# Kernel optimization log

Measured on AMD Instinct MI355X. Metric: run time of the kernel, lower is better.

The kernel has to match this reference:

```python
import jax, jax.numpy as jnp
import numpy as np

KS = 7       # neighborhood kernel size (fixed in __init__)
HEADS = 8    # num_heads (fixed in __init__)
LN_EPS = 1e-5


def _nbr_idx(L, k):
    # NATTEN-style clamped window: window start shifts inward at borders (no padding)
    starts = jnp.clip(jnp.arange(L) - k // 2, 0, L - k)
    idx = starts[:, None] + jnp.arange(k)            # [L, k] absolute neighbor coords
    rel = idx - jnp.arange(L)[:, None] + (k - 1)     # [L, k] rel-pos-bias index in [0, 2k-2]
    return idx, rel


def _na2d(x, qkv_w, qkv_b, proj_w, proj_b, rpb):
    # x: [B, H, W, C]  -> neighborhood attention with clamped 7x7 windows
    B, H, W, C = x.shape
    hd = C // HEADS
    qkv = x @ qkv_w.T + qkv_b                        # [B,H,W,3C]
    q, k, v = jnp.split(qkv, 3, axis=-1)
    q = q.reshape(B, H, W, HEADS, hd) * (hd ** -0.5)
    k = k.reshape(B, H, W, HEADS, hd)
    v = v.reshape(B, H, W, HEADS, hd)
    ri, rri = _nbr_idx(H, KS)                        # [H,KS]
    ci, rci = _nbr_idx(W, KS)                        # [W,KS]
    # gather neighborhoods: [B,H,W,KS,KS,heads,hd]
    kn = k[:, ri[:, None, :, None], ci[None, :, None, :]]
    vn = v[:, ri[:, None, :, None], ci[None, :, None, :]]
    scores = jnp.einsum('bijhd,bijpqhd->bhijpq', q, kn)   # [B,heads,H,W,KS,KS]
    bias = rpb[:, rri[:, None, :, None], rci[None, :, None, :]]  # [heads,H,W,KS,KS]
    scores = scores + bias[None]
    attn = jax.nn.softmax(scores.reshape(B, HEADS, H, W, KS * KS), axis=-1)
    vn = vn.reshape(B, H, W, KS * KS, HEADS, hd)
    out = jnp.einsum('bhijp,bijphd->bijhd', attn, vn)      # [B,H,W,heads,hd]
    out = out.reshape(B, H, W, C)
    return out @ proj_w.T + proj_b


def _layernorm(x, g, b):
    mu = jnp.mean(x, axis=-1, keepdims=True)
    var = jnp.mean((x - mu) ** 2, axis=-1, keepdims=True)
    return (x - mu) * jax.lax.rsqrt(var + LN_EPS) * g + b


def setup_inputs() -> dict:
    key = jax.random.key(0)
    ks = jax.random.split(key, 4)
    B, T, H, W, C = 2, 8, 48, 48, 64
    return {
        'q': jax.random.normal(ks[0], (B, T, H, W, C), dtype=jnp.float32),
        'qkv_w': jax.random.normal(ks[1], (3 * C, C), dtype=jnp.float32) * 0.02,
        'qkv_b': jnp.zeros((3 * C,), jnp.float32),
        'proj_w': jax.random.normal(ks[2], (C, C), dtype=jnp.float32) * 0.02,
        'proj_b': jnp.zeros((C,), jnp.float32),
        'rpb': jax.random.normal(ks[3], (HEADS, 2 * KS - 1, 2 * KS - 1), dtype=jnp.float32) * 0.02,
        'ln_g': jnp.ones((C,), jnp.float32),
        'ln_b': jnp.zeros((C,), jnp.float32),
    }


def reference(q, qkv_w, qkv_b, proj_w, proj_b, rpb, ln_g, ln_b):
    B, T, H, W, C = q.shape
    x = q.reshape(B * T, H, W, C)                    # '(b t) h w c'
    x = _na2d(x, qkv_w, qkv_b, proj_w, proj_b, rpb)  # wPT path
    x = x.reshape(B, T, H, W, C)
    return _layernorm(x, ln_g, ln_b)                 # norm_q; wGC=False
```

## Files before the change

### kernel.cpp

```cpp
#include <hip/hip_runtime.h>
#include <hip/hip_bf16.h>

#define IH   48
#define IW   48
#define CH   64
#define KS   7
#define LN_EPS 1e-5f
#define QSCALE 0.35355339059327373f
#define L2E    1.4426950408889634f

#define TS   8
#define HS   14
#define HP   196
#define KVS  136
#define AOS  72

typedef __bf16 bf16_t;
typedef bf16_t bf16x8 __attribute__((ext_vector_type(8)));
typedef float  f32x4  __attribute__((ext_vector_type(4)));
typedef float  f32x2  __attribute__((ext_vector_type(2)));

__device__ __forceinline__ float bflo(unsigned u) { union { unsigned i; float f; } v; v.i = u << 16; return v.f; }
__device__ __forceinline__ float bfhi(unsigned u) { union { unsigned i; float f; } v; v.i = u & 0xffff0000u; return v.f; }
__device__ __forceinline__ f32x2 unp2(unsigned u) { f32x2 r; r.x = bflo(u); r.y = bfhi(u); return r; }

__device__ __forceinline__ float4 ldf4u(const float* p) {
    float4 r; __builtin_memcpy(&r, p, 16); return r;
}

__device__ __forceinline__ bf16x8 pack_bf16x8(float4 lo, float4 hi) {
    bf16x8 r;
    r[0] = (bf16_t)lo.x; r[1] = (bf16_t)lo.y; r[2] = (bf16_t)lo.z; r[3] = (bf16_t)lo.w;
    r[4] = (bf16_t)hi.x; r[5] = (bf16_t)hi.y; r[6] = (bf16_t)hi.z; r[7] = (bf16_t)hi.w;
    return r;
}

__global__ __launch_bounds__(512, 4) void fused_na_kernel(
        const float* __restrict__ x,
        const float* __restrict__ w,
        const float* __restrict__ b,
        const float* __restrict__ rpb,
        const float* __restrict__ pw,
        const float* __restrict__ pb,
        const float* __restrict__ g,
        const float* __restrict__ beta,
        float* __restrict__ out) {
    __shared__ __align__(16) __hip_bfloat16 kv[HP * KVS];
    __shared__ __align__(16) __hip_bfloat16 qao[64 * AOS];

    const int blk  = blockIdx.x;
    const int n    = blk & 15;
    const int tile = blk >> 4;
    const int i0   = (tile / 6) * TS;
    const int j0   = (tile % 6) * TS;
    int h0 = i0 - 3; h0 = h0 < 0 ? 0 : (h0 > IH - HS ? IH - HS : h0);
    int w0 = j0 - 3; w0 = w0 < 0 ? 0 : (w0 > IW - HS ? IW - HS : w0);
    const int tid = threadIdx.x;
    const size_t img = (size_t)n * (IH * IW);

    {
        const int wv = tid >> 6;
        const int l  = tid & 63;
        const int m  = l & 15;
        const int kg = l >> 4;

        if (wv < 4) {
            const int ch_base = m * 4;
            const float4 bias4 = *(const float4*)(b + ch_base);
            bf16x8 wb0[4], wb1[4];
            #pragma unroll
            for (int t = 0; t < 4; ++t) {
                const float* wr_ = w + (size_t)(ch_base + t) * CH + kg * 8;
                wb0[t] = pack_bf16x8(*(const float4*)(wr_),      *(const float4*)(wr_ + 4));
                wb1[t] = pack_bf16x8(*(const float4*)(wr_ + 32), *(const float4*)(wr_ + 36));
            }
            const int px = wv * 16 + m;
            const int hr = i0 + (px >> 3);
            const int wc = j0 + (px & 7);
            const float* xr = x + (img + hr * IW + wc) * CH + kg * 8;
            const bf16x8 a0 = pack_bf16x8(*(const float4*)(xr),      *(const float4*)(xr + 4));
            const bf16x8 a1 = pack_bf16x8(*(const float4*)(xr + 32), *(const float4*)(xr + 36));
            float val[4][4];
            #pragma unroll
            for (int t = 0; t < 4; ++t) {
                f32x4 acc = {0.f, 0.f, 0.f, 0.f};
                acc = __builtin_amdgcn_mfma_f32_16x16x32_bf16(a0, wb0[t], acc, 0, 0, 0);
                acc = __builtin_amdgcn_mfma_f32_16x16x32_bf16(a1, wb1[t], acc, 0, 0, 0);
                const float bias = (t == 0) ? bias4.x : (t == 1) ? bias4.y : (t == 2) ? bias4.z : bias4.w;
                #pragma unroll
                for (int rr = 0; rr < 4; ++rr) val[t][rr] = (acc[rr] + bias) * (QSCALE * L2E);
            }
            #pragma unroll
            for (int rr = 0; rr < 4; ++rr) {
                const int pix = wv * 16 + kg * 4 + rr;
                union { ushort4 u; __hip_bfloat16 hh[4]; } pk;
                #pragma unroll
                for (int t = 0; t < 4; ++t) pk.hh[t] = __float2bfloat16(val[t][rr]);
                *reinterpret_cast<ushort4*>(qao + pix * AOS + ch_base) = pk.u;
            }
        }

        {
            const int grp = 1 + (wv >> 2);
            const int ch_base = grp * 64 + m * 4;
            const float4 bias4 = *(const float4*)(b + ch_base);
            bf16x8 wb0[4], wb1[4];
            #pragma unroll
            for (int t = 0; t < 4; ++t) {
                const float* wr_ = w + (size_t)(ch_base + t) * CH + kg * 8;
                wb0[t] = pack_bf16x8(*(const float4*)(wr_),      *(const float4*)(wr_ + 4));
                wb1[t] = pack_bf16x8(*(const float4*)(wr_ + 32), *(const float4*)(wr_ + 36));
            }
            for (int mt = wv & 3; mt < 13; mt += 4) {
                int hp = mt * 16 + m; if (hp > HP - 1) hp = HP - 1;
                const int hr = h0 + hp / HS;
                const int wc = w0 + hp % HS;
                const float* xr = x + (img + hr * IW + wc) * CH + kg * 8;
                const bf16x8 a0 = pack_bf16x8(*(const float4*)(xr),      *(const float4*)(xr + 4));
                const bf16x8 a1 = pack_bf16x8(*(const float4*)(xr + 32), *(const float4*)(xr + 36));
                float val[4][4];
                #pragma unroll
                for (int t = 0; t < 4; ++t) {
                    f32x4 acc = {0.f, 0.f, 0.f, 0.f};
                    acc = __builtin_amdgcn_mfma_f32_16x16x32_bf16(a0, wb0[t], acc, 0, 0, 0);
                    acc = __builtin_amdgcn_mfma_f32_16x16x32_bf16(a1, wb1[t], acc, 0, 0, 0);
                    const float bias = (t == 0) ? bias4.x : (t == 1) ? bias4.y : (t == 2) ? bias4.z : bias4.w;
                    #pragma unroll
                    for (int rr = 0; rr < 4; ++rr) val[t][rr] = acc[rr] + bias;
                }
                #pragma unroll
                for (int rr = 0; rr < 4; ++rr) {
                    const int pix = mt * 16 + kg * 4 + rr;
                    if (pix < HP) {
                        union { ushort4 u; __hip_bfloat16 hh[4]; } pk;
                        #pragma unroll
                        for (int t = 0; t < 4; ++t) pk.hh[t] = __float2bfloat16(val[t][rr]);
                        *reinterpret_cast<ushort4*>(kv + pix * KVS + (grp - 1) * 64 + m * 4) = pk.u;
                    }
                }
            }
        }
    }
    __syncthreads();

    {
        const int h  = tid & 7;
        const int px = tid >> 3;
        const int i  = i0 + (px >> 3);
        const int j  = j0 + (px & 7);

        f32x2 q0[4];
        {
            const uint4 u = *reinterpret_cast<const uint4*>(qao + px * AOS + h * 8);
            q0[0] = unp2(u.x); q0[1] = unp2(u.y); q0[2] = unp2(u.z); q0[3] = unp2(u.w);
        }
        __syncthreads();

        int si = i - 3;  si = si < 0 ? 0 : (si > IH - KS ? IH - KS : si);
        int sj = j - 3;  sj = sj < 0 ? 0 : (sj > IW - KS ? IW - KS : sj);
        const float* rpc = rpb + h * (2*KS-1) * (2*KS-1)
                               + (si - i + (KS-1)) * (2*KS-1) + (sj - j + (KS-1));
        const __hip_bfloat16* kbase = kv + ((si - h0) * HS + (sj - w0)) * KVS + h * 8;

        float lr = 0.f;
        f32x2 a[4];
        #pragma unroll
        for (int d = 0; d < 4; ++d) a[d] = (f32x2){0.f, 0.f};

        #pragma unroll
        for (int p = 0; p < KS; ++p) {
            const __hip_bfloat16* row = kbase + p * (HS * KVS);
            uint4 kb[KS], vb[KS];
            #pragma unroll
            for (int qq = 0; qq < KS; ++qq) {
                kb[qq] = *reinterpret_cast<const uint4*>(row + qq * KVS);
                vb[qq] = *reinterpret_cast<const uint4*>(row + qq * KVS + 64);
            }
            const float* rr = rpc + p * (2*KS-1);
            const float4 ba = ldf4u(rr);
            const float4 bb = ldf4u(rr + 3);

            float s[KS];
            #pragma unroll
            for (int qq = 0; qq < KS; ++qq) {
                const f32x2 k0 = unp2(kb[qq].x), k1 = unp2(kb[qq].y);
                const f32x2 k2 = unp2(kb[qq].z), k3 = unp2(kb[qq].w);
                f32x2 t = q0[0]*k0 + q0[1]*k1 + q0[2]*k2 + q0[3]*k3;
                s[qq] = t.x + t.y;
            }
            float e[KS];
            e[0] = __builtin_amdgcn_exp2f(fmaf(ba.x, L2E, s[0]));
            e[1] = __builtin_amdgcn_exp2f(fmaf(ba.y, L2E, s[1]));
            e[2] = __builtin_amdgcn_exp2f(fmaf(ba.z, L2E, s[2]));
            e[3] = __builtin_amdgcn_exp2f(fmaf(ba.w, L2E, s[3]));
            e[4] = __builtin_amdgcn_exp2f(fmaf(bb.y, L2E, s[4]));
            e[5] = __builtin_amdgcn_exp2f(fmaf(bb.z, L2E, s[5]));
            e[6] = __builtin_amdgcn_exp2f(fmaf(bb.w, L2E, s[6]));

            #pragma unroll
            for (int qq = 0; qq < KS; ++qq) {
                const f32x2 v0 = unp2(vb[qq].x), v1 = unp2(vb[qq].y);
                const f32x2 v2 = unp2(vb[qq].z), v3 = unp2(vb[qq].w);
                lr += e[qq];
                a[0] += e[qq] * v0; a[1] += e[qq] * v1;
                a[2] += e[qq] * v2; a[3] += e[qq] * v3;
            }
        }
        const float inv = 1.f / lr;
        union { uint4 u; __hip_bfloat16 hh[8]; } pk;
        #pragma unroll
        for (int d = 0; d < 4; ++d) {
            pk.hh[2*d]   = __float2bfloat16(a[d].x * inv);
            pk.hh[2*d+1] = __float2bfloat16(a[d].y * inv);
        }
        *reinterpret_cast<uint4*>(qao + px * AOS + h * 8) = pk.u;
    }
    __syncthreads();

    if ((tid >> 6) < 4) {
        const int wv = tid >> 6;
        const int l  = tid & 63;
        const int m  = l & 15;
        const int kg = l >> 4;

        const __hip_bfloat16* ar = qao + (wv * 16 + m) * AOS + kg * 8;
        const bf16x8 a0 = *reinterpret_cast<const bf16x8*>(ar);
        const bf16x8 a1 = *reinterpret_cast<const bf16x8*>(ar + 32);

        const int ch_base = m * 4;
        const float4 bias4 = *(const float4*)(pb + ch_base);

        float val[4][4];
        #pragma unroll
        for (int t = 0; t < 4; ++t) {
            const float* wr_ = pw + (size_t)(ch_base + t) * CH + kg * 8;
            const bf16x8 b0 = pack_bf16x8(*(const float4*)(wr_),      *(const float4*)(wr_ + 4));
            const bf16x8 b1 = pack_bf16x8(*(const float4*)(wr_ + 32), *(const float4*)(wr_ + 36));
            f32x4 acc = {0.f, 0.f, 0.f, 0.f};
            acc = __builtin_amdgcn_mfma_f32_16x16x32_bf16(a0, b0, acc, 0, 0, 0);
            acc = __builtin_amdgcn_mfma_f32_16x16x32_bf16(a1, b1, acc, 0, 0, 0);
            const float bias = (t == 0) ? bias4.x : (t == 1) ? bias4.y : (t == 2) ? bias4.z : bias4.w;
            #pragma unroll
            for (int r = 0; r < 4; ++r) val[t][r] = acc[r] + bias;
        }

        float sm[4];
        #pragma unroll
        for (int r = 0; r < 4; ++r) sm[r] = val[0][r] + val[1][r] + val[2][r] + val[3][r];
        #pragma unroll
        for (int mask = 1; mask <= 8; mask <<= 1) {
            #pragma unroll
            for (int r = 0; r < 4; ++r) sm[r] += __shfl_xor(sm[r], mask, 64);
        }
        float mu[4];
        #pragma unroll
        for (int r = 0; r < 4; ++r) mu[r] = sm[r] * (1.f / 64.f);

        float qs[4];
        #pragma unroll
        for (int r = 0; r < 4; ++r) {
            float aa = val[0][r] - mu[r], bq = val[1][r] - mu[r];
            float c  = val[2][r] - mu[r], d  = val[3][r] - mu[r];
            qs[r] = aa * aa + bq * bq + c * c + d * d;
        }
        #pragma unroll
        for (int mask = 1; mask <= 8; mask <<= 1) {
            #pragma unroll
            for (int r = 0; r < 4; ++r) qs[r] += __shfl_xor(qs[r], mask, 64);
        }
        float rs[4];
        #pragma unroll
        for (int r = 0; r < 4; ++r) rs[r] = rsqrtf(qs[r] * (1.f / 64.f) + LN_EPS);

        const float4 g4  = *(const float4*)(g + ch_base);
        const float4 be4 = *(const float4*)(beta + ch_base);
        #pragma unroll
        for (int r = 0; r < 4; ++r) {
            const int pl = wv * 16 + kg * 4 + r;
            const int gi = i0 + (pl >> 3), gj = j0 + (pl & 7);
            float4 o;
            o.x = (val[0][r] - mu[r]) * rs[r] * g4.x + be4.x;
            o.y = (val[1][r] - mu[r]) * rs[r] * g4.y + be4.y;
            o.z = (val[2][r] - mu[r]) * rs[r] * g4.z + be4.z;
            o.w = (val[3][r] - mu[r]) * rs[r] * g4.w + be4.w;
            *reinterpret_cast<float4*>(out + (img + gi * IW + gj) * CH + ch_base) = o;
        }
    }
}

extern "C" void kernel_launch(void* const* d_in, const int* in_sizes, int n_in,
                              void* d_out, int out_size, void* d_ws, size_t ws_size,
                              hipStream_t stream) {
    const float* x      = (const float*)d_in[0];
    const float* qkv_w  = (const float*)d_in[1];
    const float* qkv_b  = (const float*)d_in[2];
    const float* proj_w = (const float*)d_in[3];
    const float* proj_b = (const float*)d_in[4];
    const float* rpb    = (const float*)d_in[5];
    const float* ln_g   = (const float*)d_in[6];
    const float* ln_b   = (const float*)d_in[7];
    float* out = (float*)d_out;

    fused_na_kernel<<<576, 512, 0, stream>>>(x, qkv_w, qkv_b, rpb,
                                             proj_w, proj_b, ln_g, ln_b, out);
}
```

Before: 119.9 us.

## Retile to 6x12 output tiles with 576-thread blocks and LDS-staged rpb

Changes the spatial tile from 8x8 to 6x12 pixels, so the K/V halo grows from 14x14 to 12x18 while covering 72 outputs, which lowers halo recompute per output pixel. The grid becomes 512 blocks of 576 threads. A dedicated ninth wave computes Q while the other eight compute K/V, and the relative-position bias table is copied into shared memory instead of being read from global memory per neighbor row. The neighbor-row loop is no longer unrolled, and the projection and LayerNorm stage now uses five waves with padding guards, which adds some idle lanes and more LDS use per block.

```diff
diff --git a/kernel.cpp b/kernel.cpp
--- a/kernel.cpp
+++ b/kernel.cpp
@@ -9,11 +9,15 @@
 #define QSCALE 0.35355339059327373f
 #define L2E    1.4426950408889634f
 
-#define TS   8
-#define HS   14
-#define HP   196
+#define TSH  6
+#define TSW  12
+#define TPX  72
+#define HSH  12
+#define HSW  18
+#define HP   216
 #define KVS  136
 #define AOS  72
+#define RPBN 1352
 
 typedef __bf16 bf16_t;
 typedef bf16_t bf16x8 __attribute__((ext_vector_type(8)));
@@ -23,10 +27,6 @@
 __device__ __forceinline__ float bflo(unsigned u) { union { unsigned i; float f; } v; v.i = u << 16; return v.f; }
 __device__ __forceinline__ float bfhi(unsigned u) { union { unsigned i; float f; } v; v.i = u & 0xffff0000u; return v.f; }
 __device__ __forceinline__ f32x2 unp2(unsigned u) { f32x2 r; r.x = bflo(u); r.y = bfhi(u); return r; }
-
-__device__ __forceinline__ float4 ldf4u(const float* p) {
-    float4 r; __builtin_memcpy(&r, p, 16); return r;
-}
 
 __device__ __forceinline__ bf16x8 pack_bf16x8(float4 lo, float4 hi) {
     bf16x8 r;
@@ -35,7 +35,7 @@
     return r;
 }
 
-__global__ __launch_bounds__(512, 4) void fused_na_kernel(
+__global__ __launch_bounds__(576, 5) void fused_na_kernel(
         const float* __restrict__ x,
         const float* __restrict__ w,
         const float* __restrict__ b,
@@ -46,17 +46,20 @@
         const float* __restrict__ beta,
         float* __restrict__ out) {
     __shared__ __align__(16) __hip_bfloat16 kv[HP * KVS];
-    __shared__ __align__(16) __hip_bfloat16 qao[64 * AOS];
+    __shared__ __align__(16) __hip_bfloat16 qao[TPX * AOS];
+    __shared__ __align__(16) float rpbl[RPBN];
 
     const int blk  = blockIdx.x;
     const int n    = blk & 15;
     const int tile = blk >> 4;
-    const int i0   = (tile / 6) * TS;
-    const int j0   = (tile % 6) * TS;
-    int h0 = i0 - 3; h0 = h0 < 0 ? 0 : (h0 > IH - HS ? IH - HS : h0);
-    int w0 = j0 - 3; w0 = w0 < 0 ? 0 : (w0 > IW - HS ? IW - HS : w0);
+    const int i0   = (tile >> 2) * TSH;
+    const int j0   = (tile & 3) * TSW;
+    int h0 = i0 - 3; h0 = h0 < 0 ? 0 : (h0 > IH - HSH ? IH - HSH : h0);
+    int w0 = j0 - 3; w0 = w0 < 0 ? 0 : (w0 > IW - HSW ? IW - HSW : w0);
     const int tid = threadIdx.x;
     const size_t img = (size_t)n * (IH * IW);
+
+    for (int idx = tid; idx < RPBN; idx += 576) rpbl[idx] = rpb[idx];
 
     {
         const int wv = tid >> 6;
@@ -64,7 +67,7 @@
         const int m  = l & 15;
         const int kg = l >> 4;
 
-        if (wv < 4) {
+        if (wv == 8) {
             const int ch_base = m * 4;
             const float4 bias4 = *(const float4*)(b + ch_base);
             bf16x8 wb0[4], wb1[4];
@@ -74,34 +77,37 @@
                 wb0[t] = pack_bf16x8(*(const float4*)(wr_),      *(const float4*)(wr_ + 4));
                 wb1[t] = pack_bf16x8(*(const float4*)(wr_ + 32), *(const float4*)(wr_ + 36));
             }
-            const int px = wv * 16 + m;
-            const int hr = i0 + (px >> 3);
-            const int wc = j0 + (px & 7);
-            const float* xr = x + (img + hr * IW + wc) * CH + kg * 8;
-            const bf16x8 a0 = pack_bf16x8(*(const float4*)(xr),      *(const float4*)(xr + 4));
-            const bf16x8 a1 = pack_bf16x8(*(const float4*)(xr + 32), *(const float4*)(xr + 36));
-            float val[4][4];
-            #pragma unroll
-            for (int t = 0; t < 4; ++t) {
-                f32x4 acc = {0.f, 0.f, 0.f, 0.f};
-                acc = __builtin_amdgcn_mfma_f32_16x16x32_bf16(a0, wb0[t], acc, 0, 0, 0);
-                acc = __builtin_amdgcn_mfma_f32_16x16x32_bf16(a1, wb1[t], acc, 0, 0, 0);
-                const float bias = (t == 0) ? bias4.x : (t == 1) ? bias4.y : (t == 2) ? bias4.z : bias4.w;
+            for (int mt = 0; mt < 5; ++mt) {
+                int px = mt * 16 + m; if (px > TPX - 1) px = TPX - 1;
+                const int hr = i0 + px / TSW;
+                const int wc = j0 + px % TSW;
+                const float* xr = x + (img + hr * IW + wc) * CH + kg * 8;
+                const bf16x8 a0 = pack_bf16x8(*(const float4*)(xr),      *(const float4*)(xr + 4));
+                const bf16x8 a1 = pack_bf16x8(*(const float4*)(xr + 32), *(const float4*)(xr + 36));
+                float val[4][4];
                 #pragma unroll
-                for (int rr = 0; rr < 4; ++rr) val[t][rr] = (acc[rr] + bias) * (QSCALE * L2E);
-            }
-            #pragma unroll
-            for (int rr = 0; rr < 4; ++rr) {
-                const int pix = wv * 16 + kg * 4 + rr;
-                union { ushort4 u; __hip_bfloat16 hh[4]; } pk;
+                for (int t = 0; t < 4; ++t) {
+                    f32x4 acc = {0.f, 0.f, 0.f, 0.f};
+                    acc = __builtin_amdgcn_mfma_f32_16x16x32_bf16(a0, wb0[t], acc, 0, 0, 0);
+                    acc = __builtin_amdgcn_mfma_f32_16x16x32_bf16(a1, wb1[t], acc, 0, 0, 0);
+                    const float bias = (t == 0) ? bias4.x : (t == 1) ? bias4.y : (t == 2) ? bias4.z : bias4.w;
+                    #pragma unroll
+                    for (int rr = 0; rr < 4; ++rr) val[t][rr] = (acc[rr] + bias) * (QSCALE * L2E);
+                }
                 #pragma unroll
-                for (int t = 0; t < 4; ++t) pk.hh[t] = __float2bfloat16(val[t][rr]);
-                *reinterpret_cast<ushort4*>(qao + pix * AOS + ch_base) = pk.u;
-            }
-        }
-
-        {
+                for (int rr = 0; rr < 4; ++rr) {
+                    const int pix = mt * 16 + kg * 4 + rr;
+                    if (pix < TPX) {
+                        union { ushort4 u; __hip_bfloat16 hh[4]; } pk;
+                        #pragma unroll
+                        for (int t = 0; t < 4; ++t) pk.hh[t] = __float2bfloat16(val[t][rr]);
+                        *reinterpret_cast<ushort4*>(qao + pix * AOS + ch_base) = pk.u;
+                    }
+                }
+            }
+        } else {
             const int grp = 1 + (wv >> 2);
+            const int wg  = wv & 3;
             const int ch_base = grp * 64 + m * 4;
             const float4 bias4 = *(const float4*)(b + ch_base);
             bf16x8 wb0[4], wb1[4];
@@ -111,10 +117,10 @@
                 wb0[t] = pack_bf16x8(*(const float4*)(wr_),      *(const float4*)(wr_ + 4));
                 wb1[t] = pack_bf16x8(*(const float4*)(wr_ + 32), *(const float4*)(wr_ + 36));
             }
-            for (int mt = wv & 3; mt < 13; mt += 4) {
+            for (int mt = wg; mt < 14; mt += 4) {
                 int hp = mt * 16 + m; if (hp > HP - 1) hp = HP - 1;
-                const int hr = h0 + hp / HS;
-                const int wc = w0 + hp % HS;
+                const int hr = h0 + hp / HSW;
+                const int wc = w0 + hp % HSW;
                 const float* xr = x + (img + hr * IW + wc) * CH + kg * 8;
                 const bf16x8 a0 = pack_bf16x8(*(const float4*)(xr),      *(const float4*)(xr + 4));
                 const bf16x8 a1 = pack_bf16x8(*(const float4*)(xr + 32), *(const float4*)(xr + 36));
@@ -146,8 +152,8 @@
     {
         const int h  = tid & 7;
         const int px = tid >> 3;
-        const int i  = i0 + (px >> 3);
-        const int j  = j0 + (px & 7);
+        const int i  = i0 + px / TSW;
+        const int j  = j0 + px % TSW;
 
         f32x2 q0[4];
         {
@@ -158,27 +164,26 @@
 
         int si = i - 3;  si = si < 0 ? 0 : (si > IH - KS ? IH - KS : si);
         int sj = j - 3;  sj = sj < 0 ? 0 : (sj > IW - KS ? IW - KS : sj);
-        const float* rpc = rpb + h * (2*KS-1) * (2*KS-1)
-                               + (si - i + (KS-1)) * (2*KS-1) + (sj - j + (KS-1));
-        const __hip_bfloat16* kbase = kv + ((si - h0) * HS + (sj - w0)) * KVS + h * 8;
+        const float* rpc = rpbl + h * (2*KS-1) * (2*KS-1)
+                                + (si - i + (KS-1)) * (2*KS-1) + (sj - j + (KS-1));
+        const __hip_bfloat16* kbase = kv + ((si - h0) * HSW + (sj - w0)) * KVS + h * 8;
 
         float lr = 0.f;
         f32x2 a[4];
         #pragma unroll
         for (int d = 0; d < 4; ++d) a[d] = (f32x2){0.f, 0.f};
 
-        #pragma unroll
         for (int p = 0; p < KS; ++p) {
-            const __hip_bfloat16* row = kbase + p * (HS * KVS);
+            const __hip_bfloat16* row = kbase + p * (HSW * KVS);
             uint4 kb[KS], vb[KS];
             #pragma unroll
             for (int qq = 0; qq < KS; ++qq) {
                 kb[qq] = *reinterpret_cast<const uint4*>(row + qq * KVS);
                 vb[qq] = *reinterpret_cast<const uint4*>(row + qq * KVS + 64);
             }
-            const float* rr = rpc + p * (2*KS-1);
-            const float4 ba = ldf4u(rr);
-            const float4 bb = ldf4u(rr + 3);
+            float bl[KS];
+            #pragma unroll
+            for (int qq = 0; qq < KS; ++qq) bl[qq] = rpc[p * (2*KS-1) + qq];
 
             float s[KS];
             #pragma unroll
@@ -189,13 +194,9 @@
                 s[qq] = t.x + t.y;
             }
             float e[KS];
-            e[0] = __builtin_amdgcn_exp2f(fmaf(ba.x, L2E, s[0]));
-            e[1] = __builtin_amdgcn_exp2f(fmaf(ba.y, L2E, s[1]));
-            e[2] = __builtin_amdgcn_exp2f(fmaf(ba.z, L2E, s[2]));
-            e[3] = __builtin_amdgcn_exp2f(fmaf(ba.w, L2E, s[3]));
-            e[4] = __builtin_amdgcn_exp2f(fmaf(bb.y, L2E, s[4]));
-            e[5] = __builtin_amdgcn_exp2f(fmaf(bb.z, L2E, s[5]));
-            e[6] = __builtin_amdgcn_exp2f(fmaf(bb.w, L2E, s[6]));
+            #pragma unroll
+            for (int qq = 0; qq < KS; ++qq)
+                e[qq] = __builtin_amdgcn_exp2f(fmaf(bl[qq], L2E, s[qq]));
 
             #pragma unroll
             for (int qq = 0; qq < KS; ++qq) {
@@ -217,13 +218,14 @@
     }
     __syncthreads();
 
-    if ((tid >> 6) < 4) {
+    if ((tid >> 6) < 5) {
         const int wv = tid >> 6;
         const int l  = tid & 63;
         const int m  = l & 15;
         const int kg = l >> 4;
 
-        const __hip_bfloat16* ar = qao + (wv * 16 + m) * AOS + kg * 8;
+        int ap = wv * 16 + m; if (ap > TPX - 1) ap = TPX - 1;
+        const __hip_bfloat16* ar = qao + ap * AOS + kg * 8;
         const bf16x8 a0 = *reinterpret_cast<const bf16x8*>(ar);
         const bf16x8 a1 = *reinterpret_cast<const bf16x8*>(ar + 32);
 
@@ -277,13 +279,15 @@
         #pragma unroll
         for (int r = 0; r < 4; ++r) {
             const int pl = wv * 16 + kg * 4 + r;
-            const int gi = i0 + (pl >> 3), gj = j0 + (pl & 7);
-            float4 o;
-            o.x = (val[0][r] - mu[r]) * rs[r] * g4.x + be4.x;
-            o.y = (val[1][r] - mu[r]) * rs[r] * g4.y + be4.y;
-            o.z = (val[2][r] - mu[r]) * rs[r] * g4.z + be4.z;
-            o.w = (val[3][r] - mu[r]) * rs[r] * g4.w + be4.w;
-            *reinterpret_cast<float4*>(out + (img + gi * IW + gj) * CH + ch_base) = o;
+            if (pl < TPX) {
+                const int gi = i0 + pl / TSW, gj = j0 + pl % TSW;
+                float4 o;
+                o.x = (val[0][r] - mu[r]) * rs[r] * g4.x + be4.x;
+                o.y = (val[1][r] - mu[r]) * rs[r] * g4.y + be4.y;
+                o.z = (val[2][r] - mu[r]) * rs[r] * g4.z + be4.z;
+                o.w = (val[3][r] - mu[r]) * rs[r] * g4.w + be4.w;
+                *reinterpret_cast<float4*>(out + (img + gi * IW + gj) * CH + ch_base) = o;
+            }
         }
     }
 }
@@ -301,6 +305,6 @@
     const float* ln_b   = (const float*)d_in[7];
     float* out = (float*)d_out;
 
-    fused_na_kernel<<<576, 512, 0, stream>>>(x, qkv_w, qkv_b, rpb,
+    fused_na_kernel<<<512, 576, 0, stream>>>(x, qkv_w, qkv_b, rpb,
                                              proj_w, proj_b, ln_g, ln_b, out);
 }
```

Result: faster. 115.6 us (-3.6%).
